# Kernel tuning notes

Hardware: AMD Instinct MI355X
Metric: run time of the kernel (lower is better)

## Reference

```python
import jax, jax.numpy as jnp
import numpy as np

B, S, D_MODEL = 4, 2048, 1024
H, DK, DV = 16, 64, 64
MASKED = False


def setup_inputs() -> dict:
    key = jax.random.key(0)
    ks = jax.random.split(key, 7)
    return {
        "q": jax.random.normal(ks[0], (B, S, D_MODEL), dtype=jnp.float32),
        "k": jax.random.normal(ks[1], (B, S, D_MODEL), dtype=jnp.float32),
        "v": jax.random.normal(ks[2], (B, S, D_MODEL), dtype=jnp.float32),
        "Wq": jax.random.normal(ks[3], (H, D_MODEL, DK), dtype=jnp.float32) * 0.05,
        "Wk": jax.random.normal(ks[4], (H, D_MODEL, DK), dtype=jnp.float32) * 0.05,
        "Wv": jax.random.normal(ks[5], (H, D_MODEL, DV), dtype=jnp.float32) * 0.05,
        "Wo": jax.random.normal(ks[6], (H * DV, D_MODEL), dtype=jnp.float32) * 0.05,
    }


def reference(q, k, v, Wq, Wk, Wv, Wo):
    # Per-head projections, batched over heads instead of a Python loop.
    Q = jnp.einsum("bsd,hdk->bhsk", q, Wq)  # [B,H,S,Dk]
    K = jnp.einsum("btd,hdk->bhtk", k, Wk)  # [B,H,S,Dk]
    V = jnp.einsum("btd,hdv->bhtv", v, Wv)  # [B,H,S,Dv]

    scale = 1.0 / jnp.sqrt(jnp.asarray(DK, dtype=Q.dtype))
    scores = jnp.einsum("bhsk,bhtk->bhst", Q, K) * scale  # [B,H,S,S]
    if MASKED:
        causal = jnp.tril(jnp.ones((S, S), dtype=bool))
        scores = jnp.where(causal, scores, jnp.finfo(scores.dtype).min)
    attn = jax.nn.softmax(scores, axis=-1)
    heads = jnp.einsum("bhst,bhtv->bhsv", attn, V)  # [B,H,S,Dv]

    # concat heads along feature dim (tf.concat(heads, axis=-1)) then Wo projection
    multi = heads.transpose(0, 2, 1, 3).reshape(q.shape[0], q.shape[1], H * DV)
    return multi @ Wo  # [B,S,D_MODEL]
```

## Files before the change

### kernel.cpp

```cpp
#include <hip/hip_runtime.h>
#include <hip/hip_bf16.h>

typedef __attribute__((ext_vector_type(8))) short short8;
typedef __attribute__((ext_vector_type(4))) short short4v;
typedef __attribute__((ext_vector_type(4))) float f32x4;
typedef __attribute__((ext_vector_type(2))) float f32x2;
typedef __attribute__((ext_vector_type(4))) unsigned short us4;
typedef __attribute__((ext_vector_type(2))) unsigned int u32x2;

#define NB 4
#define SEQ 2048
#define DMODEL 1024
#define NH 16
#define DHEAD 64
#define QSCALE 0.18033688011112042f
#define FM 34.0f

static __device__ __forceinline__ unsigned short f2bf(float f) {
    __hip_bfloat16 h = __float2bfloat16(f);
    return *reinterpret_cast<unsigned short*>(&h);
}
static __device__ __forceinline__ unsigned int cvt_pk(float lo, float hi) {
    float2 t; t.x = lo; t.y = hi;
    __hip_bfloat162 h = __float22bfloat162_rn(t);
    return *reinterpret_cast<unsigned int*>(&h);
}

typedef __attribute__((address_space(3))) unsigned int lds_u32_t;
typedef __attribute__((address_space(1))) const unsigned int glob_u32_t;
static __device__ __forceinline__ void gl_lds16(const unsigned short* g, unsigned short* l) {
    __builtin_amdgcn_global_load_lds((glob_u32_t*)g, (lds_u32_t*)l, 16, 0, 0);
}

__global__ __launch_bounds__(256) void prep_all(const float* __restrict__ q,
                                                const float* __restrict__ k,
                                                const float* __restrict__ v,
                                                const float* __restrict__ wq,
                                                const float* __restrict__ wk,
                                                const float* __restrict__ wv,
                                                const float* __restrict__ wo,
                                                unsigned short* __restrict__ xq,
                                                unsigned short* __restrict__ xk,
                                                unsigned short* __restrict__ xv,
                                                unsigned short* __restrict__ oq,
                                                unsigned short* __restrict__ ok,
                                                unsigned short* __restrict__ ov,
                                                unsigned short* __restrict__ oo) {
    const int z = blockIdx.y;
    int i = blockIdx.x * 256 + threadIdx.x;
    if (z < 3) {
        const float* in = z == 0 ? q : (z == 1 ? k : v);
        unsigned short* out = z == 0 ? xq : (z == 1 ? xk : xv);
        f32x4 val = ((const f32x4*)in)[i];
        u32x2 o;
        o.x = cvt_pk(val.x, val.y);
        o.y = cvt_pk(val.z, val.w);
        ((u32x2*)out)[i] = o;
    } else {
        if (i >= NH * DMODEL * DHEAD) return;
        if (z < 6) {
            const float* w = z == 3 ? wq : (z == 4 ? wk : wv);
            unsigned short* out = z == 3 ? oq : (z == 4 ? ok : ov);
            float scale = z == 3 ? QSCALE : 1.0f;
            int kk = i & 63;
            int d  = (i >> 6) & 1023;
            int h  = i >> 16;
            out[(size_t)(h * 64 + kk) * DMODEL + d] = f2bf(w[i] * scale);
        } else {
            int c = i & 1023;
            int r = i >> 10;
            oo[(size_t)c * 1024 + r] = f2bf(wo[i]);
        }
    }
}

struct GemmAcc { f32x4 a[4][4]; };

static __device__ __forceinline__ void gemm_core(const unsigned short* __restrict__ A,
                                                 const unsigned short* __restrict__ Bt,
                                                 unsigned short (*As)[4096],
                                                 unsigned short (*Bs)[4096],
                                                 int m0, int n0, int K, GemmAcc& acc) {
    const int tid = threadIdx.x;
    const int w = tid >> 6, l = tid & 63;
    const int lane16 = l & 15, quad = l >> 4;
    const int wr = w >> 1, wc = w & 1;

#pragma unroll
    for (int a = 0; a < 4; a++)
#pragma unroll
        for (int b = 0; b < 4; b++) acc.a[a][b] = (f32x4){0.f, 0.f, 0.f, 0.f};

    const int i0 = 2 * w, i1 = 2 * w + 1;
    const int rs = l >> 2;
    const int cc = ((l & 3) ^ ((l >> 3) & 3)) * 8;
    const unsigned short* a0 = A + (size_t)(m0 + i0 * 16 + rs) * K + cc;
    const unsigned short* a1 = A + (size_t)(m0 + i1 * 16 + rs) * K + cc;
    const unsigned short* b0 = Bt + (size_t)(n0 + i0 * 16 + rs) * K + cc;
    const unsigned short* b1 = Bt + (size_t)(n0 + i1 * 16 + rs) * K + cc;

    const int cl = (quad ^ ((lane16 >> 1) & 3)) * 8;
    const int ra = (wr * 64 + lane16) * 32 + cl;
    const int rb = (wc * 64 + lane16) * 32 + cl;

    for (int k0 = 0; k0 < K; k0 += 64) {
        __syncthreads();
#pragma unroll
        for (int h = 0; h < 2; h++) {
            gl_lds16(a0 + k0 + h * 32, &As[h][i0 * 512]);
            gl_lds16(a1 + k0 + h * 32, &As[h][i1 * 512]);
            gl_lds16(b0 + k0 + h * 32, &Bs[h][i0 * 512]);
            gl_lds16(b1 + k0 + h * 32, &Bs[h][i1 * 512]);
        }
        __syncthreads();
#pragma unroll
        for (int h = 0; h < 2; h++) {
            short8 af[4], bf[4];
#pragma unroll
            for (int mt = 0; mt < 4; mt++) af[mt] = *(const short8*)&As[h][ra + mt * 512];
#pragma unroll
            for (int nt = 0; nt < 4; nt++) bf[nt] = *(const short8*)&Bs[h][rb + nt * 512];
#pragma unroll
            for (int mt = 0; mt < 4; mt++)
#pragma unroll
                for (int nt = 0; nt < 4; nt++)
                    acc.a[mt][nt] = __builtin_amdgcn_mfma_f32_16x16x32_bf16(
                        af[mt], bf[nt], acc.a[mt][nt], 0, 0, 0);
        }
    }
}

__global__ __launch_bounds__(256) void gemm_qkv(const unsigned short* __restrict__ xq,
                                                const unsigned short* __restrict__ xk,
                                                const unsigned short* __restrict__ xv,
                                                const unsigned short* __restrict__ wq,
                                                const unsigned short* __restrict__ wk,
                                                const unsigned short* __restrict__ wv,
                                                unsigned short* __restrict__ Qb,
                                                unsigned short* __restrict__ Kb,
                                                unsigned short* __restrict__ Vtb) {
    __shared__ unsigned short As[2][4096];
    __shared__ unsigned short Bs[2][4096];
    const int z = blockIdx.z;
    const unsigned short* A = z == 0 ? xq : (z == 1 ? xk : xv);
    const unsigned short* Bt = z == 0 ? wq : (z == 1 ? wk : wv);
    unsigned short* out = z == 0 ? Qb : (z == 1 ? Kb : Vtb);

    const int m0 = blockIdx.x * 128, n0 = blockIdx.y * 128;
    GemmAcc acc;
    gemm_core(A, Bt, As, Bs, m0, n0, DMODEL, acc);

    const int l = threadIdx.x & 63, w = threadIdx.x >> 6;
    const int lane16 = l & 15, quad = l >> 4;
    const int wr = w >> 1, wc = w & 1;
    if (z < 2) {
#pragma unroll
        for (int mt = 0; mt < 4; mt++)
#pragma unroll
            for (int nt = 0; nt < 4; nt++)
#pragma unroll
                for (int r = 0; r < 4; r++) {
                    int m = m0 + wr * 64 + mt * 16 + quad * 4 + r;
                    int n = n0 + wc * 64 + nt * 16 + lane16;
                    int b_ = m >> 11, s = m & 2047, h = n >> 6, kk = n & 63;
                    out[((size_t)((b_ * NH + h) * SEQ + s) << 6) + kk] = f2bf(acc.a[mt][nt][r]);
                }
    } else {
#pragma unroll
        for (int mt = 0; mt < 4; mt++)
#pragma unroll
            for (int nt = 0; nt < 4; nt++) {
                int m = m0 + wr * 64 + mt * 16 + quad * 4;
                int n = n0 + wc * 64 + nt * 16 + lane16;
                int b_ = m >> 11, s = m & 2047, h = n >> 6, kk = n & 63;
                u32x2 pk;
                pk.x = cvt_pk(acc.a[mt][nt][0], acc.a[mt][nt][1]);
                pk.y = cvt_pk(acc.a[mt][nt][2], acc.a[mt][nt][3]);
                *(u32x2*)&out[(size_t)((b_ * NH + h) * DHEAD + kk) * SEQ + s] = pk;
            }
    }
}

__global__ __launch_bounds__(256) void gemm_out(const unsigned short* __restrict__ A,
                                                const unsigned short* __restrict__ Bt,
                                                float* __restrict__ C) {
    __shared__ unsigned short As[2][4096];
    __shared__ unsigned short Bs[2][4096];
    const int m0 = blockIdx.x * 128, n0 = blockIdx.y * 128;
    GemmAcc acc;
    gemm_core(A, Bt, As, Bs, m0, n0, DMODEL, acc);

    const int l = threadIdx.x & 63, w = threadIdx.x >> 6;
    const int lane16 = l & 15, quad = l >> 4;
    const int wr = w >> 1, wc = w & 1;
#pragma unroll
    for (int mt = 0; mt < 4; mt++)
#pragma unroll
        for (int nt = 0; nt < 4; nt++)
#pragma unroll
            for (int r = 0; r < 4; r++) {
                int m = m0 + wr * 64 + mt * 16 + quad * 4 + r;
                int n = n0 + wc * 64 + nt * 16 + lane16;
                C[(size_t)m * DMODEL + n] = acc.a[mt][nt][r];
            }
}

__global__ __launch_bounds__(256) void flash_attn(const unsigned short* __restrict__ Q,
                                                  const unsigned short* __restrict__ Kg,
                                                  const unsigned short* __restrict__ Vt,
                                                  unsigned short* __restrict__ Hout) {
    __shared__ unsigned short Ks[2][4096];
    __shared__ unsigned short Vs[2][4096];

    const int tid = threadIdx.x;
    const int w = tid >> 6, l = tid & 63;
    const int lane16 = l & 15, quad = l >> 4;
    const int wg = ((blockIdx.x & 7) << 7) | (blockIdx.x >> 3);
    const int bh = wg >> 4, b_ = bh >> 4, h = bh & 15;
    const int s0 = (wg & 15) * 128;

    const unsigned short* Qbh = Q + (size_t)bh * SEQ * DHEAD;
    const unsigned short* Kbh = Kg + (size_t)bh * SEQ * DHEAD;
    const unsigned short* Vbh = Vt + (size_t)bh * DHEAD * SEQ;

    short8 qf[2][2];
#pragma unroll
    for (int qm = 0; qm < 2; qm++)
#pragma unroll
        for (int ks = 0; ks < 2; ks++)
            qf[qm][ks] = *(const short8*)(Qbh +
                (size_t)(s0 + w * 32 + qm * 16 + lane16) * DHEAD + ks * 32 + quad * 8);

    f32x4 o[2][4];
#pragma unroll
    for (int qm = 0; qm < 2; qm++)
#pragma unroll
        for (int dt = 0; dt < 4; dt++) o[qm][dt] = (f32x4){0.f, 0.f, 0.f, 0.f};
    f32x2 lsum2[2];
    lsum2[0] = (f32x2){0.f, 0.f};
    lsum2[1] = (f32x2){0.f, 0.f};
    const f32x4 scinit = (f32x4){-FM, -FM, -FM, -FM};

    const int i0 = 2 * w, i1 = 2 * w + 1;
    const int rs = l >> 3;
    const int cgs = ((l & 7) ^ rs) * 8;
    const unsigned short* kg0 = Kbh + (size_t)(i0 * 8 + rs) * DHEAD + cgs;
    const unsigned short* kg1 = Kbh + (size_t)(i1 * 8 + rs) * DHEAD + cgs;
    const unsigned short* vg0 = Vbh + (size_t)(i0 * 8 + rs) * SEQ + cgs;
    const unsigned short* vg1 = Vbh + (size_t)(i1 * 8 + rs) * SEQ + cgs;

    const int swz = lane16 & 7;

#define STAGE(B, T)                                            \
    do {                                                       \
        const size_t ko_ = (size_t)(T) * (64 * DHEAD);         \
        const int vo_ = (T) * 64;                              \
        gl_lds16(kg0 + ko_, &Ks[B][i0 * 512]);                 \
        gl_lds16(kg1 + ko_, &Ks[B][i1 * 512]);                 \
        gl_lds16(vg0 + vo_, &Vs[B][i0 * 512]);                 \
        gl_lds16(vg1 + vo_, &Vs[B][i1 * 512]);                 \
    } while (0)

    auto compute = [&](const unsigned short* kb, const unsigned short* vb) {
        short4v pf[2][4];
#pragma unroll
        for (int nt = 0; nt < 4; nt++) {
            const int kbase = (nt * 16 + lane16) * 64;
            short8 kf0 = *(const short8*)&kb[kbase + ((quad ^ swz) * 8)];
            short8 kf1 = *(const short8*)&kb[kbase + (((4 + quad) ^ swz) * 8)];
#pragma unroll
            for (int qm = 0; qm < 2; qm++) {
                f32x4 sc = __builtin_amdgcn_mfma_f32_16x16x32_bf16(kf0, qf[qm][0], scinit, 0, 0, 0);
                sc = __builtin_amdgcn_mfma_f32_16x16x32_bf16(kf1, qf[qm][1], sc, 0, 0, 0);
                float p0 = __builtin_amdgcn_exp2f(sc.x);
                float p1 = __builtin_amdgcn_exp2f(sc.y);
                float p2 = __builtin_amdgcn_exp2f(sc.z);
                float p3 = __builtin_amdgcn_exp2f(sc.w);
                f32x2 pa; pa.x = p0; pa.y = p1;
                f32x2 pb; pb.x = p2; pb.y = p3;
                lsum2[qm] += pa;
                lsum2[qm] += pb;
                u32x2 pk;
                pk.x = cvt_pk(p0, p1);
                pk.y = cvt_pk(p2, p3);
                pf[qm][nt] = __builtin_bit_cast(short4v, pk);
            }
        }
#pragma unroll
        for (int nt = 0; nt < 4; nt++) {
#pragma unroll
            for (int dt = 0; dt < 4; dt++) {
                int cl = (2 * nt + (quad >> 1)) ^ swz;
                short4v vf = *(const short4v*)&vb[(dt * 16 + lane16) * 64 + cl * 8 + (quad & 1) * 4];
                o[0][dt] = __builtin_amdgcn_mfma_f32_16x16x16bf16_1k(vf, pf[0][nt], o[0][dt], 0, 0, 0);
                o[1][dt] = __builtin_amdgcn_mfma_f32_16x16x16bf16_1k(vf, pf[1][nt], o[1][dt], 0, 0, 0);
            }
        }
    };

    STAGE(0, 0);
    asm volatile("s_waitcnt vmcnt(0)" ::: "memory");
    __builtin_amdgcn_s_barrier();

    const int NT = SEQ / 64;
    for (int t = 0; t < NT; t += 2) {
        STAGE(1, t + 1);
        asm volatile("" ::: "memory");
        compute(Ks[0], Vs[0]);
        asm volatile("" ::: "memory");
        asm volatile("s_waitcnt vmcnt(0)" ::: "memory");
        __builtin_amdgcn_s_barrier();

        if (t + 2 < NT) STAGE(0, t + 2);
        asm volatile("" ::: "memory");
        compute(Ks[1], Vs[1]);
        asm volatile("" ::: "memory");
        asm volatile("s_waitcnt vmcnt(0)" ::: "memory");
        __builtin_amdgcn_s_barrier();
    }
#undef STAGE

    float lsum[2];
#pragma unroll
    for (int qm = 0; qm < 2; qm++) {
        float s = lsum2[qm].x + lsum2[qm].y;
        s += __shfl_xor(s, 16);
        s += __shfl_xor(s, 32);
        lsum[qm] = s;
    }
#pragma unroll
    for (int qm = 0; qm < 2; qm++) {
        float inv = 1.f / lsum[qm];
        int s = s0 + w * 32 + qm * 16 + lane16;
        size_t rowbase = (size_t)(b_ * SEQ + s) * DMODEL + h * 64;
#pragma unroll
        for (int dt = 0; dt < 4; dt++) {
            u32x2 ov;
            ov.x = cvt_pk(o[qm][dt][0] * inv, o[qm][dt][1] * inv);
            ov.y = cvt_pk(o[qm][dt][2] * inv, o[qm][dt][3] * inv);
            *(u32x2*)&Hout[rowbase + dt * 16 + quad * 4] = ov;
        }
    }
}

extern "C" void kernel_launch(void* const* d_in, const int* in_sizes, int n_in,
                              void* d_out, int out_size, void* d_ws, size_t ws_size,
                              hipStream_t stream) {
    const float* q  = (const float*)d_in[0];
    const float* k  = (const float*)d_in[1];
    const float* v  = (const float*)d_in[2];
    const float* Wq = (const float*)d_in[3];
    const float* Wk = (const float*)d_in[4];
    const float* Wv = (const float*)d_in[5];
    const float* Wo = (const float*)d_in[6];

    const size_t SZ_X = (size_t)NB * SEQ * DMODEL * 2;
    const size_t SZ_W = (size_t)DMODEL * DMODEL * 2;
    char* ws = (char*)d_ws;
    unsigned short* xq  = (unsigned short*)(ws);
    unsigned short* xk  = (unsigned short*)(ws + SZ_X);
    unsigned short* xv  = (unsigned short*)(ws + 2 * SZ_X);
    unsigned short* wqt = (unsigned short*)(ws + 3 * SZ_X);
    unsigned short* wkt = (unsigned short*)(ws + 3 * SZ_X + SZ_W);
    unsigned short* wvt = (unsigned short*)(ws + 3 * SZ_X + 2 * SZ_W);
    unsigned short* wot = (unsigned short*)(ws + 3 * SZ_X + 3 * SZ_W);
    unsigned short* Qb  = (unsigned short*)(ws + 3 * SZ_X + 4 * SZ_W);
    unsigned short* Kb  = (unsigned short*)(ws + 4 * SZ_X + 4 * SZ_W);
    unsigned short* Vtb = (unsigned short*)(ws + 5 * SZ_X + 4 * SZ_W);
    unsigned short* hd  = (unsigned short*)(ws + 6 * SZ_X + 4 * SZ_W);
    if (ws_size < 7 * SZ_X + 4 * SZ_W) return;

    const int n4 = NB * SEQ * DMODEL / 4;
    prep_all<<<dim3(n4 / 256, 7), 256, 0, stream>>>(q, k, v, Wq, Wk, Wv, Wo,
                                                    xq, xk, xv, wqt, wkt, wvt, wot);

    const int M = NB * SEQ;
    gemm_qkv<<<dim3(M / 128, DMODEL / 128, 3), 256, 0, stream>>>(
        xq, xk, xv, wqt, wkt, wvt, Qb, Kb, Vtb);

    flash_attn<<<dim3((SEQ / 128) * NB * NH), 256, 0, stream>>>(Qb, Kb, Vtb, hd);

    gemm_out<<<dim3(M / 128, DMODEL / 128), 256, 0, stream>>>(hd, wot, (float*)d_out);
}
```

Before: 355.3 us.

## Switch flash attention to 32x32x16 MFMA tiles with permlane32 swap for P

Rewrites the attention inner loop to use 32x32x16 bf16 MFMA for both QK^T and PV instead of 16x16 tiles. P values are repacked into the B-operand layout in registers with v_permlane32_swap, which avoids an LDS round trip. This cuts the MFMA instruction count and the number of LDS fragment reads per tile, and changes the register layout of accumulators and the output store pattern. It risks higher register pressure and new bank-conflict patterns in the LDS reads.

Result: no change. 356.0 us (+0.2%).

```diff
diff --git a/kernel.cpp b/kernel.cpp
--- a/kernel.cpp
+++ b/kernel.cpp
@@ -4,9 +4,11 @@
 typedef __attribute__((ext_vector_type(8))) short short8;
 typedef __attribute__((ext_vector_type(4))) short short4v;
 typedef __attribute__((ext_vector_type(4))) float f32x4;
+typedef __attribute__((ext_vector_type(16))) float f32x16;
 typedef __attribute__((ext_vector_type(2))) float f32x2;
 typedef __attribute__((ext_vector_type(4))) unsigned short us4;
 typedef __attribute__((ext_vector_type(2))) unsigned int u32x2;
+typedef __attribute__((ext_vector_type(4))) unsigned int u32x4;
 
 #define NB 4
 #define SEQ 2048
@@ -30,6 +32,10 @@
 typedef __attribute__((address_space(1))) const unsigned int glob_u32_t;
 static __device__ __forceinline__ void gl_lds16(const unsigned short* g, unsigned short* l) {
     __builtin_amdgcn_global_load_lds((glob_u32_t*)g, (lds_u32_t*)l, 16, 0, 0);
+}
+
+static __device__ __forceinline__ void pl32swap(unsigned& a, unsigned& b) {
+    asm("v_permlane32_swap_b32 %0, %1" : "+v"(a), "+v"(b));
 }
 
 __global__ __launch_bounds__(256) void prep_all(const float* __restrict__ q,
@@ -214,7 +220,7 @@
 
     const int tid = threadIdx.x;
     const int w = tid >> 6, l = tid & 63;
-    const int lane16 = l & 15, quad = l >> 4;
+    const int l31 = l & 31, hi = l >> 5;
     const int wg = ((blockIdx.x & 7) << 7) | (blockIdx.x >> 3);
     const int bh = wg >> 4, b_ = bh >> 4, h = bh & 15;
     const int s0 = (wg & 15) * 128;
@@ -223,23 +229,21 @@
     const unsigned short* Kbh = Kg + (size_t)bh * SEQ * DHEAD;
     const unsigned short* Vbh = Vt + (size_t)bh * DHEAD * SEQ;
 
-    short8 qf[2][2];
-#pragma unroll
-    for (int qm = 0; qm < 2; qm++)
-#pragma unroll
-        for (int ks = 0; ks < 2; ks++)
-            qf[qm][ks] = *(const short8*)(Qbh +
-                (size_t)(s0 + w * 32 + qm * 16 + lane16) * DHEAD + ks * 32 + quad * 8);
-
-    f32x4 o[2][4];
-#pragma unroll
-    for (int qm = 0; qm < 2; qm++)
-#pragma unroll
-        for (int dt = 0; dt < 4; dt++) o[qm][dt] = (f32x4){0.f, 0.f, 0.f, 0.f};
-    f32x2 lsum2[2];
-    lsum2[0] = (f32x2){0.f, 0.f};
-    lsum2[1] = (f32x2){0.f, 0.f};
-    const f32x4 scinit = (f32x4){-FM, -FM, -FM, -FM};
+    short8 qf[4];
+    {
+        const unsigned short* qp = Qbh + (size_t)(s0 + w * 32 + l31) * DHEAD + hi * 8;
+#pragma unroll
+        for (int dk = 0; dk < 4; dk++) qf[dk] = *(const short8*)(qp + dk * 16);
+    }
+
+    f32x16 o0, o1, scinit;
+#pragma unroll
+    for (int r = 0; r < 16; r++) { o0[r] = 0.f; o1[r] = 0.f; scinit[r] = -FM; }
+    f32x2 lsum2 = (f32x2){0.f, 0.f};
+
+    int offs[4];
+#pragma unroll
+    for (int i = 0; i < 4; i++) offs[i] = l31 * 64 + ((((i << 1) + hi) ^ (l31 & 7)) << 3);
 
     const int i0 = 2 * w, i1 = 2 * w + 1;
     const int rs = l >> 3;
@@ -248,8 +252,6 @@
     const unsigned short* kg1 = Kbh + (size_t)(i1 * 8 + rs) * DHEAD + cgs;
     const unsigned short* vg0 = Vbh + (size_t)(i0 * 8 + rs) * SEQ + cgs;
     const unsigned short* vg1 = Vbh + (size_t)(i1 * 8 + rs) * SEQ + cgs;
-
-    const int swz = lane16 & 7;
 
 #define STAGE(B, T)                                            \
     do {                                                       \
@@ -262,38 +264,40 @@
     } while (0)
 
     auto compute = [&](const unsigned short* kb, const unsigned short* vb) {
-        short4v pf[2][4];
-#pragma unroll
-        for (int nt = 0; nt < 4; nt++) {
-            const int kbase = (nt * 16 + lane16) * 64;
-            short8 kf0 = *(const short8*)&kb[kbase + ((quad ^ swz) * 8)];
-            short8 kf1 = *(const short8*)&kb[kbase + (((4 + quad) ^ swz) * 8)];
-#pragma unroll
-            for (int qm = 0; qm < 2; qm++) {
-                f32x4 sc = __builtin_amdgcn_mfma_f32_16x16x32_bf16(kf0, qf[qm][0], scinit, 0, 0, 0);
-                sc = __builtin_amdgcn_mfma_f32_16x16x32_bf16(kf1, qf[qm][1], sc, 0, 0, 0);
-                float p0 = __builtin_amdgcn_exp2f(sc.x);
-                float p1 = __builtin_amdgcn_exp2f(sc.y);
-                float p2 = __builtin_amdgcn_exp2f(sc.z);
-                float p3 = __builtin_amdgcn_exp2f(sc.w);
-                f32x2 pa; pa.x = p0; pa.y = p1;
-                f32x2 pb; pb.x = p2; pb.y = p3;
-                lsum2[qm] += pa;
-                lsum2[qm] += pb;
-                u32x2 pk;
-                pk.x = cvt_pk(p0, p1);
-                pk.y = cvt_pk(p2, p3);
-                pf[qm][nt] = __builtin_bit_cast(short4v, pk);
+#pragma unroll
+        for (int tc = 0; tc < 2; tc++) {
+            short8 kf0 = *(const short8*)(kb + tc * 2048 + offs[0]);
+            short8 kf1 = *(const short8*)(kb + tc * 2048 + offs[1]);
+            short8 kf2 = *(const short8*)(kb + tc * 2048 + offs[2]);
+            short8 kf3 = *(const short8*)(kb + tc * 2048 + offs[3]);
+            f32x16 sc = __builtin_amdgcn_mfma_f32_32x32x16_bf16(kf0, qf[0], scinit, 0, 0, 0);
+            sc = __builtin_amdgcn_mfma_f32_32x32x16_bf16(kf1, qf[1], sc, 0, 0, 0);
+            sc = __builtin_amdgcn_mfma_f32_32x32x16_bf16(kf2, qf[2], sc, 0, 0, 0);
+            sc = __builtin_amdgcn_mfma_f32_32x32x16_bf16(kf3, qf[3], sc, 0, 0, 0);
+            float p[16];
+#pragma unroll
+            for (int r = 0; r < 16; r++) p[r] = __builtin_amdgcn_exp2f(sc[r]);
+#pragma unroll
+            for (int r = 0; r < 16; r += 2) {
+                f32x2 t; t.x = p[r]; t.y = p[r + 1];
+                lsum2 += t;
             }
-        }
-#pragma unroll
-        for (int nt = 0; nt < 4; nt++) {
-#pragma unroll
-            for (int dt = 0; dt < 4; dt++) {
-                int cl = (2 * nt + (quad >> 1)) ^ swz;
-                short4v vf = *(const short4v*)&vb[(dt * 16 + lane16) * 64 + cl * 8 + (quad & 1) * 4];
-                o[0][dt] = __builtin_amdgcn_mfma_f32_16x16x16bf16_1k(vf, pf[0][nt], o[0][dt], 0, 0, 0);
-                o[1][dt] = __builtin_amdgcn_mfma_f32_16x16x16bf16_1k(vf, pf[1][nt], o[1][dt], 0, 0, 0);
+#pragma unroll
+            for (int ntp = 0; ntp < 2; ntp++) {
+                const int nt = tc * 2 + ntp;
+                unsigned c0 = cvt_pk(p[8 * ntp + 0], p[8 * ntp + 1]);
+                unsigned c1 = cvt_pk(p[8 * ntp + 2], p[8 * ntp + 3]);
+                unsigned c2 = cvt_pk(p[8 * ntp + 4], p[8 * ntp + 5]);
+                unsigned c3 = cvt_pk(p[8 * ntp + 6], p[8 * ntp + 7]);
+                pl32swap(c0, c2);
+                pl32swap(c1, c3);
+                u32x4 pk4;
+                pk4.x = c0; pk4.y = c1; pk4.z = c2; pk4.w = c3;
+                const short8 pbv = __builtin_bit_cast(short8, pk4);
+                short8 vf0 = *(const short8*)(vb + offs[nt]);
+                short8 vf1 = *(const short8*)(vb + 2048 + offs[nt]);
+                o0 = __builtin_amdgcn_mfma_f32_32x32x16_bf16(vf0, pbv, o0, 0, 0, 0);
+                o1 = __builtin_amdgcn_mfma_f32_32x32x16_bf16(vf1, pbv, o1, 0, 0, 0);
             }
         }
     };
@@ -320,26 +324,20 @@
     }
 #undef STAGE
 
-    float lsum[2];
-#pragma unroll
-    for (int qm = 0; qm < 2; qm++) {
-        float s = lsum2[qm].x + lsum2[qm].y;
-        s += __shfl_xor(s, 16);
-        s += __shfl_xor(s, 32);
-        lsum[qm] = s;
-    }
-#pragma unroll
-    for (int qm = 0; qm < 2; qm++) {
-        float inv = 1.f / lsum[qm];
-        int s = s0 + w * 32 + qm * 16 + lane16;
-        size_t rowbase = (size_t)(b_ * SEQ + s) * DMODEL + h * 64;
-#pragma unroll
-        for (int dt = 0; dt < 4; dt++) {
-            u32x2 ov;
-            ov.x = cvt_pk(o[qm][dt][0] * inv, o[qm][dt][1] * inv);
-            ov.y = cvt_pk(o[qm][dt][2] * inv, o[qm][dt][3] * inv);
-            *(u32x2*)&Hout[rowbase + dt * 16 + quad * 4] = ov;
-        }
+    float lsv = lsum2.x + lsum2.y;
+    lsv += __shfl_xor(lsv, 32);
+    const float inv = 1.f / lsv;
+    const int s = s0 + w * 32 + l31;
+    unsigned short* hp = Hout + (size_t)(b_ * SEQ + s) * DMODEL + h * 64 + hi * 4;
+#pragma unroll
+    for (int g = 0; g < 4; g++) {
+        u32x2 ov;
+        ov.x = cvt_pk(o0[4 * g + 0] * inv, o0[4 * g + 1] * inv);
+        ov.y = cvt_pk(o0[4 * g + 2] * inv, o0[4 * g + 3] * inv);
+        *(u32x2*)(hp + g * 8) = ov;
+        ov.x = cvt_pk(o1[4 * g + 0] * inv, o1[4 * g + 1] * inv);
+        ov.y = cvt_pk(o1[4 * g + 2] * inv, o1[4 * g + 3] * inv);
+        *(u32x2*)(hp + 32 + g * 8) = ov;
     }
 }
 
```
